# Kernel tuning notes

Measured on AMD Instinct MI355X. Metric: run time of the kernel, lower is better.

## Reference

```python
import jax, jax.numpy as jnp
import numpy as np

NEG_SLOPE = 0.2
EPS = 1e-16  # PyG softmax eps


def _gat_conv(x, src, dst, W, att_src, att_dst, bias, heads, out_ch):
    """PyG GATConv (eval mode, self-loops already appended, concat output)."""
    N = x.shape[0]
    xw = (x @ W).reshape(N, heads, out_ch)            # [N,H,C]
    a_src = jnp.sum(xw * att_src, axis=-1)            # [N,H]
    a_dst = jnp.sum(xw * att_dst, axis=-1)            # [N,H]
    e = jax.nn.leaky_relu(a_src[src] + a_dst[dst], NEG_SLOPE)  # [E,H]
    m = jax.ops.segment_max(e, dst, num_segments=N)   # [N,H] (self-loops -> no empty segs)
    e = jnp.exp(e - m[dst])
    denom = jax.ops.segment_sum(e, dst, num_segments=N)
    alpha = e / (denom[dst] + EPS)                    # [E,H]
    msg = xw[src] * alpha[:, :, None]                 # [E,H,C]
    out = jax.ops.segment_sum(msg, dst, num_segments=N)  # [N,H,C]
    return out.reshape(N, heads * out_ch) + bias


def setup_inputs() -> dict:
    key = jax.random.key(0)
    ks = jax.random.split(key, 12)
    N, E, F_in, H, C, NC = 20000, 320000, 512, 8, 64, 32
    x = jax.random.normal(ks[0], (N, F_in), dtype=jnp.float32)
    edge_index = jax.random.randint(ks[1], (2, E), 0, N, dtype=jnp.int64)
    g = lambda k, shape, fan: jax.random.normal(k, shape, dtype=jnp.float32) * (1.0 / np.sqrt(fan))
    return {
        "x": x,
        "edge_index": edge_index,
        "W1": g(ks[2], (F_in, H * C), F_in),
        "att_src1": g(ks[3], (H, C), C),
        "att_dst1": g(ks[4], (H, C), C),
        "b1": jnp.zeros((H * C,), dtype=jnp.float32),
        "W2": g(ks[5], (H * C, NC), H * C),
        "att_src2": g(ks[6], (1, NC), NC),
        "att_dst2": g(ks[7], (1, NC), NC),
        "b2": jnp.zeros((NC,), dtype=jnp.float32),
    }


def reference(x, edge_index, W1, att_src1, att_dst1, b1, W2, att_src2, att_dst2, b2):
    N = x.shape[0]
    H, C = att_src1.shape
    NC = att_src2.shape[1]
    # GATConv adds self-loops by default
    loops = jnp.arange(N, dtype=edge_index.dtype)
    src = jnp.concatenate([edge_index[0], loops])
    dst = jnp.concatenate([edge_index[1], loops])
    h = _gat_conv(x, src, dst, W1, att_src1, att_dst1, b1, H, C)
    h = jax.nn.elu(h)
    h = _gat_conv(h, src, dst, W2, att_src2, att_dst2, b2, 1, NC)
    return jax.nn.log_softmax(h, axis=1)
```

## Files before the change

kernel.cpp:

```cpp
#include <hip/hip_runtime.h>
#include <math.h>

#define NEG_SLOPE 0.2f
#define SM_EPS 1e-16f

typedef short short8 __attribute__((ext_vector_type(8)));
typedef float floatx4 __attribute__((ext_vector_type(4)));


__device__ inline unsigned short f2bf(float x) {
    unsigned int u = __float_as_uint(x);
    unsigned int r = (u + 0x7FFFu + ((u >> 16) & 1u)) >> 16;
    return (unsigned short)r;
}

__device__ inline float bf2f(unsigned short h) {
    return __uint_as_float(((unsigned int)h) << 16);
}

__device__ inline float bflo(unsigned int u) { return __uint_as_float(u << 16); }
__device__ inline float bfhi(unsigned int u) { return __uint_as_float(u & 0xFFFF0000u); }

__device__ __forceinline__ void gl_lds16(const unsigned short* g, unsigned short* l) {
    __builtin_amdgcn_global_load_lds(
        (const __attribute__((address_space(1))) unsigned int*)(g),
        (__attribute__((address_space(3))) unsigned int*)(l), 16, 0, 0);
}

__device__ inline void get_edge(const int* __restrict__ srcA, const int* __restrict__ dstA,
                                int e, int E, int& s, int& d) {
    if (e < E) { s = srcA[e]; d = dstA[e]; }
    else { s = e - E; d = e - E; }
}


__global__ __launch_bounds__(256) void k_prep(const float* __restrict__ x,
                                              unsigned short* __restrict__ xb,
                                              const float* __restrict__ W1,
                                              unsigned short* __restrict__ w1t,
                                              const float* __restrict__ W2,
                                              unsigned short* __restrict__ w2bt,
                                              const int* __restrict__ dstA,
                                              int E, int Ep,
                                              int* __restrict__ deg,
                                              int nblk_deg, int nblk_x) {
    __shared__ float tile[32][33];
    int bx = blockIdx.x;
    int t = threadIdx.x;
    if (bx < nblk_deg) {
        int e = bx * 256 + t;
        if (e < Ep) {
            int d = (e < E) ? dstA[e] : (e - E);
            atomicAdd(&deg[d], 1);
        }
    } else if (bx < nblk_deg + nblk_x) {
        int i = ((bx - nblk_deg) * 256 + t) * 4;
        float4 v = *(const float4*)(x + i);
        ushort4 o;
        o.x = f2bf(v.x); o.y = f2bf(v.y); o.z = f2bf(v.z); o.w = f2bf(v.w);
        *(ushort4*)(xb + i) = o;
    } else if (bx < nblk_deg + nblk_x + 256) {
        int b = bx - nblk_deg - nblk_x;
        int kb = (b & 15) * 32;
        int nb = (b >> 4) * 32;
        int tx = t & 31, ty = t >> 5;
        #pragma unroll
        for (int i = 0; i < 32; i += 8)
            tile[ty + i][tx] = W1[(size_t)(kb + ty + i) * 512 + nb + tx];
        __syncthreads();
        #pragma unroll
        for (int i = 0; i < 32; i += 8)
            w1t[(size_t)(nb + ty + i) * 512 + kb + tx] = f2bf(tile[tx][ty + i]);
    } else {
        int i = (bx - nblk_deg - nblk_x - 256) * 256 + t;
        int c = i >> 9, k = i & 511;
        w2bt[i] = f2bf(W2[k * 32 + c]);
    }
}


__global__ __launch_bounds__(256) void k_scan1(const int* __restrict__ deg, int* __restrict__ incl,
                                               int* __restrict__ part, int N) {
    __shared__ int sm[256];
    int t = threadIdx.x;
    int i = blockIdx.x * 256 + t;
    int v = (i < N) ? deg[i] : 0;
    sm[t] = v; __syncthreads();
    for (int o = 1; o < 256; o <<= 1) {
        int x = (t >= o) ? sm[t - o] : 0;
        __syncthreads();
        sm[t] += x;
        __syncthreads();
    }
    if (i < N) incl[i] = sm[t];
    if (t == 255) part[blockIdx.x] = sm[255];
}

__global__ __launch_bounds__(256) void k_scan3(const int* __restrict__ incl, const int* __restrict__ part,
                                               const int* __restrict__ deg, int* __restrict__ off,
                                               int* __restrict__ cursor, int N) {
    __shared__ int sm[256];
    int bx = blockIdx.x, t = threadIdx.x;
    int partial = 0;
    for (int i = t; i < bx; i += 256) partial += part[i];
    sm[t] = partial; __syncthreads();
    for (int o = 128; o > 0; o >>= 1) {
        if (t < o) sm[t] += sm[t + o];
        __syncthreads();
    }
    int base = sm[0];
    int i = bx * 256 + t;
    if (i >= N) return;
    int v = incl[i] + base;
    off[i + 1] = v;
    cursor[i] = v - deg[i];
    if (i == 0) off[0] = 0;
}

__global__ __launch_bounds__(256) void k_scatter(const int* __restrict__ srcA, const int* __restrict__ dstA,
                                                 int E, int Ep, int* __restrict__ cursor,
                                                 int* __restrict__ src_s) {
    int e = blockIdx.x * 256 + threadIdx.x;
    if (e >= Ep) return;
    int s, d; get_edge(srcA, dstA, e, E, s, d);
    int p = atomicAdd(&cursor[d], 1);
    src_s[p] = s;
}


__global__ __launch_bounds__(256) void k_gemm1_mfma(const unsigned short* __restrict__ A,
                                                    const unsigned short* __restrict__ Bt,
                                                    const float* __restrict__ att_s,
                                                    const float* __restrict__ att_d,
                                                    unsigned short* __restrict__ C,
                                                    float* __restrict__ a_sd,
                                                    float* __restrict__ a_dd, int M) {
    const int K = 512;
    __shared__ unsigned short As[128 * 32];
    __shared__ unsigned short Bs[128 * 32];
    int t = threadIdx.x;
    int lane = t & 63;
    int w = t >> 6;
    int row0 = blockIdx.x * 128;
    int col0 = blockIdx.y * 128;
    int wm = (w >> 1) * 64, wn = (w & 1) * 64;
    int l15 = lane & 15, q = lane >> 4;

    int mrow = t >> 2;
    int kk = (t & 3) * 8;
    unsigned short* ldsA0 = &As[w * 512];
    unsigned short* ldsA1 = &As[2048 + w * 512];
    unsigned short* ldsB0 = &Bs[w * 512];
    unsigned short* ldsB1 = &Bs[2048 + w * 512];

    floatx4 acc[4][4] = {};

    for (int k0 = 0; k0 < K; k0 += 32) {
        gl_lds16(A  + (size_t)(row0 + mrow) * K + k0 + kk,      ldsA0);
        gl_lds16(A  + (size_t)(row0 + 64 + mrow) * K + k0 + kk, ldsA1);
        gl_lds16(Bt + (size_t)(col0 + mrow) * K + k0 + kk,      ldsB0);
        gl_lds16(Bt + (size_t)(col0 + 64 + mrow) * K + k0 + kk, ldsB1);
        __syncthreads();
        short8 af[4], bfr[4];
        #pragma unroll
        for (int i = 0; i < 4; ++i)
            af[i] = *(const short8*)(&As[(wm + i * 16 + l15) * 32 + q * 8]);
        #pragma unroll
        for (int j = 0; j < 4; ++j)
            bfr[j] = *(const short8*)(&Bs[(wn + j * 16 + l15) * 32 + q * 8]);
        #pragma unroll
        for (int i = 0; i < 4; ++i)
            #pragma unroll
            for (int j = 0; j < 4; ++j)
                acc[i][j] = __builtin_amdgcn_mfma_f32_16x16x32_bf16(af[i], bfr[j], acc[i][j], 0, 0, 0);
        __syncthreads();
    }

    #pragma unroll
    for (int i = 0; i < 4; ++i) {
        #pragma unroll
        for (int p = 0; p < 4; ++p) {
            int r = row0 + wm + i * 16 + q * 4 + p;
            if (r < M) {
                #pragma unroll
                for (int j = 0; j < 4; ++j) {
                    int c = col0 + wn + j * 16 + l15;
                    C[(size_t)r * 512 + c] = f2bf(acc[i][j][p]);
                }
            }
        }
    }

    int hh = blockIdx.y * 2 + (w & 1);
    float asr[4], adr[4];
    #pragma unroll
    for (int j = 0; j < 4; ++j) {
        asr[j] = att_s[hh * 64 + j * 16 + l15];
        adr[j] = att_d[hh * 64 + j * 16 + l15];
    }
    #pragma unroll
    for (int i = 0; i < 4; ++i) {
        #pragma unroll
        for (int p = 0; p < 4; ++p) {
            float ds = 0.f, dd = 0.f;
            #pragma unroll
            for (int j = 0; j < 4; ++j) {
                ds = fmaf(acc[i][j][p], asr[j], ds);
                dd = fmaf(acc[i][j][p], adr[j], dd);
            }
            #pragma unroll
            for (int mk = 1; mk <= 8; mk <<= 1) {
                ds += __shfl_xor(ds, mk);
                dd += __shfl_xor(dd, mk);
            }
            int r = row0 + wm + i * 16 + q * 4 + p;
            if (l15 == 0 && r < M) {
                a_sd[r * 8 + hh] = ds;
                a_dd[r * 8 + hh] = dd;
            }
        }
    }
}


__global__ __launch_bounds__(256) void k_l1(const unsigned short* __restrict__ xw,
                                            const float* __restrict__ a_s,
                                            const float* __restrict__ a_d,
                                            const int* __restrict__ off,
                                            const int* __restrict__ src_s,
                                            const float* __restrict__ bias,
                                            unsigned short* __restrict__ hout, int N) {
    int wid = threadIdx.x >> 6, lane = threadIdx.x & 63;
    int n = blockIdx.x * 4 + wid;
    if (n >= N) return;
    int p0 = off[n], p1 = off[n + 1];
    int q = lane >> 3;
    int be = lane >> 3;
    int bh = lane & 7;
    float adb = a_d[n * 8 + bh];
    const size_t cbase = (size_t)8 * lane;

    float acc[8] = {};
    float s = 0.f;
    int p = p0;
    for (; p + 8 <= p1; p += 8) {
        int bsrc = src_s[p + be];
        float e = a_s[bsrc * 8 + bh] + adb;
        e = e > 0.f ? e : NEG_SLOPE * e;
        float w8 = __expf(e);
        #pragma unroll
        for (int j = 0; j < 8; ++j) {
            int sj = __shfl(bsrc, j * 8);
            float wj = __shfl(w8, j * 8 + q);
            const uint4 u = *(const uint4*)(xw + (size_t)sj * 512 + cbase);
            s += wj;
            acc[0] = fmaf(wj, bflo(u.x), acc[0]); acc[1] = fmaf(wj, bfhi(u.x), acc[1]);
            acc[2] = fmaf(wj, bflo(u.y), acc[2]); acc[3] = fmaf(wj, bfhi(u.y), acc[3]);
            acc[4] = fmaf(wj, bflo(u.z), acc[4]); acc[5] = fmaf(wj, bfhi(u.z), acc[5]);
            acc[6] = fmaf(wj, bflo(u.w), acc[6]); acc[7] = fmaf(wj, bfhi(u.w), acc[7]);
        }
    }
    if (p < p1) {
        int nb = p1 - p;
        int bsrc = src_s[p + (be < nb ? be : 0)];
        float e = a_s[bsrc * 8 + bh] + adb;
        e = e > 0.f ? e : NEG_SLOPE * e;
        float w8 = __expf(e);
        for (int j = 0; j < nb; ++j) {
            int sj = __shfl(bsrc, j * 8);
            float wj = __shfl(w8, j * 8 + q);
            const uint4 u = *(const uint4*)(xw + (size_t)sj * 512 + cbase);
            s += wj;
            acc[0] = fmaf(wj, bflo(u.x), acc[0]); acc[1] = fmaf(wj, bfhi(u.x), acc[1]);
            acc[2] = fmaf(wj, bflo(u.y), acc[2]); acc[3] = fmaf(wj, bfhi(u.y), acc[3]);
            acc[4] = fmaf(wj, bflo(u.z), acc[4]); acc[5] = fmaf(wj, bfhi(u.z), acc[5]);
            acc[6] = fmaf(wj, bflo(u.w), acc[6]); acc[7] = fmaf(wj, bfhi(u.w), acc[7]);
        }
    }

    float inv = 1.f / (s + SM_EPS);
    unsigned int ov[4];
    #pragma unroll
    for (int j = 0; j < 4; ++j) {
        float v0 = acc[2 * j] * inv     + bias[cbase + 2 * j];
        float v1 = acc[2 * j + 1] * inv + bias[cbase + 2 * j + 1];
        v0 = v0 > 0.f ? v0 : expm1f(v0);
        v1 = v1 > 0.f ? v1 : expm1f(v1);
        ov[j] = (unsigned int)f2bf(v0) | ((unsigned int)f2bf(v1) << 16);
    }
    *(uint4*)(hout + (size_t)n * 512 + cbase) = make_uint4(ov[0], ov[1], ov[2], ov[3]);
}


__global__ __launch_bounds__(256) void k_gemm2_mfma(const unsigned short* __restrict__ A,
                                                    const unsigned short* __restrict__ Bt,
                                                    const float* __restrict__ att_s,
                                                    const float* __restrict__ att_d,
                                                    unsigned short* __restrict__ O,
                                                    float* __restrict__ a_s, float* __restrict__ a_d,
                                                    int M) {
    const int K = 512;
    __shared__ unsigned short As[64 * 40];
    __shared__ unsigned short Bs[32 * 40];
    int t = threadIdx.x;
    int lane = t & 63;
    int w = t >> 6;
    int row0 = blockIdx.x * 64;
    int l15 = lane & 15, q = lane >> 4;

    floatx4 acc[2] = {};

    for (int k0 = 0; k0 < K; k0 += 32) {
        {
            int flat = t * 8;
            int m = flat >> 5, kk = flat & 31;
            uint4 va = make_uint4(0u, 0u, 0u, 0u);
            int gr = row0 + m;
            if (gr < M) va = *(const uint4*)(A + (size_t)gr * K + k0 + kk);
            *(uint4*)(&As[m * 40 + kk]) = va;
            if (t < 128) {
                int nn = t >> 2, kb = (t & 3) * 8;
                *(uint4*)(&Bs[nn * 40 + kb]) = *(const uint4*)(Bt + (size_t)nn * K + k0 + kb);
            }
        }
        __syncthreads();
        short8 af = *(const short8*)(&As[(w * 16 + l15) * 40 + q * 8]);
        short8 b0 = *(const short8*)(&Bs[(l15) * 40 + q * 8]);
        short8 b1 = *(const short8*)(&Bs[(16 + l15) * 40 + q * 8]);
        acc[0] = __builtin_amdgcn_mfma_f32_16x16x32_bf16(af, b0, acc[0], 0, 0, 0);
        acc[1] = __builtin_amdgcn_mfma_f32_16x16x32_bf16(af, b1, acc[1], 0, 0, 0);
        __syncthreads();
    }

    float as_lo = att_s[l15], as_hi = att_s[16 + l15];
    float ad_lo = att_d[l15], ad_hi = att_d[16 + l15];
    #pragma unroll
    for (int p = 0; p < 4; ++p) {
        int r = row0 + w * 16 + q * 4 + p;
        bool ok = r < M;
        float v0 = acc[0][p], v1 = acc[1][p];
        if (ok) {
            O[(size_t)r * 32 + l15]      = f2bf(v0);
            O[(size_t)r * 32 + 16 + l15] = f2bf(v1);
        }
        float ds = v0 * as_lo + v1 * as_hi;
        float dd = v0 * ad_lo + v1 * ad_hi;
        #pragma unroll
        for (int mk = 1; mk <= 8; mk <<= 1) {
            ds += __shfl_xor(ds, mk);
            dd += __shfl_xor(dd, mk);
        }
        if (ok && l15 == 0) { a_s[r] = ds; a_d[r] = dd; }
    }
}


__global__ __launch_bounds__(256) void k_l2(const unsigned short* __restrict__ hw2,
                                            const float* __restrict__ a_s,
                                            const float* __restrict__ a_d,
                                            const int* __restrict__ off,
                                            const int* __restrict__ src_s,
                                            const float* __restrict__ bias,
                                            float* __restrict__ outp, int N) {
    int wid = threadIdx.x >> 6, lane = threadIdx.x & 63;
    int n = blockIdx.x * 4 + wid;
    if (n >= N) return;
    int p0 = off[n], p1 = off[n + 1];
    float adv = a_d[n];
    int c = lane & 31, ep = lane >> 5;

    float acc = 0.f, s = 0.f;
    int p = p0;
    for (; p + 64 <= p1; p += 64) {
        int bsrc = src_s[p + lane];
        float e = a_s[bsrc] + adv;
        e = e > 0.f ? e : NEG_SLOPE * e;
        float w64 = __expf(e);
        #pragma unroll
        for (int j = 0; j < 64; j += 2) {
            int sj = __shfl(bsrc, j + ep);
            float wj = __shfl(w64, j + ep);
            s += wj;
            acc = fmaf(wj, bf2f(hw2[(size_t)sj * 32 + c]), acc);
        }
    }
    if (p < p1) {
        int nb = p1 - p;
        int bsrc = src_s[p + (lane < nb ? lane : 0)];
        float e = a_s[bsrc] + adv;
        e = e > 0.f ? e : NEG_SLOPE * e;
        float w64 = __expf(e);
        for (int j = 0; j < nb; j += 2) {
            int idx = j + ep;
            bool valid = idx < nb;
            int idc = valid ? idx : 0;
            int sj = __shfl(bsrc, idc);
            float wj = __shfl(w64, idc);
            if (valid) {
                s += wj;
                acc = fmaf(wj, bf2f(hw2[(size_t)sj * 32 + c]), acc);
            }
        }
    }
    acc += __shfl_xor(acc, 32);
    s   += __shfl_xor(s, 32);
    float v = acc / (s + SM_EPS) + bias[c];
    float mx = v;
    #pragma unroll
    for (int mk = 16; mk >= 1; mk >>= 1) mx = fmaxf(mx, __shfl_xor(mx, mk, 32));
    float ex = __expf(v - mx);
    float sum = ex;
    #pragma unroll
    for (int mk = 16; mk >= 1; mk >>= 1) sum += __shfl_xor(sum, mk, 32);
    if (lane < 32) outp[(size_t)n * 32 + c] = (v - mx) - __logf(sum);
}


extern "C" void kernel_launch(void* const* d_in, const int* in_sizes, int n_in,
                              void* d_out, int out_size, void* d_ws, size_t ws_size,
                              hipStream_t stream) {
    const float* x   = (const float*)d_in[0];
    const int*   ei  = (const int*)d_in[1];
    const float* W1  = (const float*)d_in[2];
    const float* as1 = (const float*)d_in[3];
    const float* ad1 = (const float*)d_in[4];
    const float* b1  = (const float*)d_in[5];
    const float* W2  = (const float*)d_in[6];
    const float* as2 = (const float*)d_in[7];
    const float* ad2 = (const float*)d_in[8];
    const float* b2  = (const float*)d_in[9];
    float* out = (float*)d_out;

    const int F = 512;
    const int N = in_sizes[0] / F;
    const int E = in_sizes[1] / 2;
    const int Ep = E + N;
    const int* srcA = ei;
    const int* dstA = ei + E;

    char* w = (char*)d_ws;
    auto alloc = [&](size_t b) -> void* {
        void* p = (void*)w;
        w += (b + 255) & ~(size_t)255;
        return p;
    };
    unsigned short* xbf  = (unsigned short*)alloc((size_t)N * 512 * 2);
    unsigned short* w1t  = (unsigned short*)alloc((size_t)512 * 512 * 2);
    unsigned short* w2bt = (unsigned short*)alloc((size_t)32 * 512 * 2);
    unsigned short* xw1  = (unsigned short*)alloc((size_t)N * 512 * 2);
    unsigned short* hbuf = (unsigned short*)alloc((size_t)N * 512 * 2);
    float* a_s1 = (float*)alloc((size_t)N * 8 * 4);
    float* a_d1 = (float*)alloc((size_t)N * 8 * 4);
    unsigned short* hw2 = (unsigned short*)alloc((size_t)N * 32 * 2);
    float* a_s2 = (float*)alloc((size_t)N * 4);
    float* a_d2 = (float*)alloc((size_t)N * 4);
    int* deg    = (int*)alloc((size_t)N * 4);
    int* incl   = (int*)alloc((size_t)N * 4);
    int* part   = (int*)alloc(256 * 4);
    int* off    = (int*)alloc((size_t)(N + 1) * 4);
    int* cursor = (int*)alloc((size_t)N * 4);
    int* src_s  = (int*)alloc((size_t)Ep * 4);

    int egrid = (Ep + 255) / 256;
    int sgrid = (N + 255) / 256;
    int ngrid4 = (N + 3) / 4;
    int nblk_x = (N * 512 / 4) / 256;
    int nblk_w2 = (32 * 512 + 255) / 256;

    hipMemsetAsync(deg, 0, (size_t)N * 4, stream);

    k_prep<<<egrid + nblk_x + 256 + nblk_w2, 256, 0, stream>>>(
        x, xbf, W1, w1t, W2, w2bt, dstA, E, Ep, deg, egrid, nblk_x);

    k_scan1<<<sgrid, 256, 0, stream>>>(deg, incl, part, N);
    k_scan3<<<sgrid, 256, 0, stream>>>(incl, part, deg, off, cursor, N);
    k_scatter<<<egrid, 256, 0, stream>>>(srcA, dstA, E, Ep, cursor, src_s);

    {
        dim3 g1((N + 127) / 128, 512 / 128);
        k_gemm1_mfma<<<g1, 256, 0, stream>>>(xbf, w1t, as1, ad1, xw1, a_s1, a_d1, N);
    }
    k_l1<<<ngrid4, 256, 0, stream>>>(xw1, a_s1, a_d1, off, src_s, b1, hbuf, N);

    k_gemm2_mfma<<<(N + 63) / 64, 256, 0, stream>>>(hbuf, w2bt, as2, ad2, hw2, a_s2, a_d2, N);
    k_l2<<<ngrid4, 256, 0, stream>>>(hw2, a_s2, a_d2, off, src_s, b2, out, N);
}
```

Baseline: 261.8 us.

## Split layer-1 aggregation per head with head-major attention scores

The attention logits a_s/a_d are now stored head-major ([H][N]) instead of node-major. The layer-1 aggregation kernel now gives each group of 8 lanes one (node, head) pair, with the head taken from blockIdx. Each lane computes its own edge weight and loads a 16-byte slice of the source row for that head, processing two edges per iteration. This removes the cross-lane shuffles and improves locality of the score gathers. In exchange, each edge's src index is loaded redundantly, each row gather is only 128 bytes per head group, and the per-lane edge loop is longer and more serial, so the load imbalance from varying degree grows.

```diff
diff --git a/kernel.cpp b/kernel.cpp
--- a/kernel.cpp
+++ b/kernel.cpp
@@ -215,8 +215,8 @@
             }
             int r = row0 + wm + i * 16 + q * 4 + p;
             if (l15 == 0 && r < M) {
-                a_sd[r * 8 + hh] = ds;
-                a_dd[r * 8 + hh] = dd;
+                a_sd[(size_t)hh * M + r] = ds;
+                a_dd[(size_t)hh * M + r] = dd;
             }
         }
     }
@@ -231,51 +231,47 @@
                                             const float* __restrict__ bias,
                                             unsigned short* __restrict__ hout, int N) {
     int wid = threadIdx.x >> 6, lane = threadIdx.x & 63;
-    int n = blockIdx.x * 4 + wid;
+    int h = blockIdx.x & 7;
+    int n = (blockIdx.x >> 3) * 32 + wid * 8 + (lane >> 3);
+    int li = lane & 7;
     if (n >= N) return;
     int p0 = off[n], p1 = off[n + 1];
-    int q = lane >> 3;
-    int be = lane >> 3;
-    int bh = lane & 7;
-    float adb = a_d[n * 8 + bh];
-    const size_t cbase = (size_t)8 * lane;
+    const float* ash = a_s + (size_t)h * N;
+    float adv = a_d[(size_t)h * N + n];
+    const size_t cbase = (size_t)h * 64 + (size_t)li * 8;
 
     float acc[8] = {};
     float s = 0.f;
     int p = p0;
-    for (; p + 8 <= p1; p += 8) {
-        int bsrc = src_s[p + be];
-        float e = a_s[bsrc * 8 + bh] + adb;
-        e = e > 0.f ? e : NEG_SLOPE * e;
-        float w8 = __expf(e);
-        #pragma unroll
-        for (int j = 0; j < 8; ++j) {
-            int sj = __shfl(bsrc, j * 8);
-            float wj = __shfl(w8, j * 8 + q);
-            const uint4 u = *(const uint4*)(xw + (size_t)sj * 512 + cbase);
-            s += wj;
-            acc[0] = fmaf(wj, bflo(u.x), acc[0]); acc[1] = fmaf(wj, bfhi(u.x), acc[1]);
-            acc[2] = fmaf(wj, bflo(u.y), acc[2]); acc[3] = fmaf(wj, bfhi(u.y), acc[3]);
-            acc[4] = fmaf(wj, bflo(u.z), acc[4]); acc[5] = fmaf(wj, bfhi(u.z), acc[5]);
-            acc[6] = fmaf(wj, bflo(u.w), acc[6]); acc[7] = fmaf(wj, bfhi(u.w), acc[7]);
-        }
+    for (; p + 2 <= p1; p += 2) {
+        int s0 = src_s[p];
+        int s1 = src_s[p + 1];
+        const uint4 u0 = *(const uint4*)(xw + (size_t)s0 * 512 + cbase);
+        const uint4 u1 = *(const uint4*)(xw + (size_t)s1 * 512 + cbase);
+        float e0 = ash[s0] + adv; e0 = e0 > 0.f ? e0 : NEG_SLOPE * e0;
+        float e1 = ash[s1] + adv; e1 = e1 > 0.f ? e1 : NEG_SLOPE * e1;
+        float w0 = __expf(e0);
+        float w1 = __expf(e1);
+        s += w0 + w1;
+        acc[0] = fmaf(w0, bflo(u0.x), acc[0]); acc[1] = fmaf(w0, bfhi(u0.x), acc[1]);
+        acc[2] = fmaf(w0, bflo(u0.y), acc[2]); acc[3] = fmaf(w0, bfhi(u0.y), acc[3]);
+        acc[4] = fmaf(w0, bflo(u0.z), acc[4]); acc[5] = fmaf(w0, bfhi(u0.z), acc[5]);
+        acc[6] = fmaf(w0, bflo(u0.w), acc[6]); acc[7] = fmaf(w0, bfhi(u0.w), acc[7]);
+        acc[0] = fmaf(w1, bflo(u1.x), acc[0]); acc[1] = fmaf(w1, bfhi(u1.x), acc[1]);
+        acc[2] = fmaf(w1, bflo(u1.y), acc[2]); acc[3] = fmaf(w1, bfhi(u1.y), acc[3]);
+        acc[4] = fmaf(w1, bflo(u1.z), acc[4]); acc[5] = fmaf(w1, bfhi(u1.z), acc[5]);
+        acc[6] = fmaf(w1, bflo(u1.w), acc[6]); acc[7] = fmaf(w1, bfhi(u1.w), acc[7]);
     }
     if (p < p1) {
-        int nb = p1 - p;
-        int bsrc = src_s[p + (be < nb ? be : 0)];
-        float e = a_s[bsrc * 8 + bh] + adb;
-        e = e > 0.f ? e : NEG_SLOPE * e;
-        float w8 = __expf(e);
-        for (int j = 0; j < nb; ++j) {
-            int sj = __shfl(bsrc, j * 8);
-            float wj = __shfl(w8, j * 8 + q);
-            const uint4 u = *(const uint4*)(xw + (size_t)sj * 512 + cbase);
-            s += wj;
-            acc[0] = fmaf(wj, bflo(u.x), acc[0]); acc[1] = fmaf(wj, bfhi(u.x), acc[1]);
-            acc[2] = fmaf(wj, bflo(u.y), acc[2]); acc[3] = fmaf(wj, bfhi(u.y), acc[3]);
-            acc[4] = fmaf(wj, bflo(u.z), acc[4]); acc[5] = fmaf(wj, bfhi(u.z), acc[5]);
-            acc[6] = fmaf(wj, bflo(u.w), acc[6]); acc[7] = fmaf(wj, bfhi(u.w), acc[7]);
-        }
+        int s0 = src_s[p];
+        const uint4 u0 = *(const uint4*)(xw + (size_t)s0 * 512 + cbase);
+        float e0 = ash[s0] + adv; e0 = e0 > 0.f ? e0 : NEG_SLOPE * e0;
+        float w0 = __expf(e0);
+        s += w0;
+        acc[0] = fmaf(w0, bflo(u0.x), acc[0]); acc[1] = fmaf(w0, bfhi(u0.x), acc[1]);
+        acc[2] = fmaf(w0, bflo(u0.y), acc[2]); acc[3] = fmaf(w0, bfhi(u0.y), acc[3]);
+        acc[4] = fmaf(w0, bflo(u0.z), acc[4]); acc[5] = fmaf(w0, bfhi(u0.z), acc[5]);
+        acc[6] = fmaf(w0, bflo(u0.w), acc[6]); acc[7] = fmaf(w0, bfhi(u0.w), acc[7]);
     }
 
     float inv = 1.f / (s + SM_EPS);
@@ -480,7 +476,10 @@
         dim3 g1((N + 127) / 128, 512 / 128);
         k_gemm1_mfma<<<g1, 256, 0, stream>>>(xbf, w1t, as1, ad1, xw1, a_s1, a_d1, N);
     }
-    k_l1<<<ngrid4, 256, 0, stream>>>(xw1, a_s1, a_d1, off, src_s, b1, hbuf, N);
+    {
+        int ngrid32 = (N + 31) / 32;
+        k_l1<<<ngrid32 * 8, 256, 0, stream>>>(xw1, a_s1, a_d1, off, src_s, b1, hbuf, N);
+    }
 
     k_gemm2_mfma<<<(N + 63) / 64, 256, 0, stream>>>(hbuf, w2bt, as2, ad2, hw2, a_s2, a_d2, N);
     k_l2<<<ngrid4, 256, 0, stream>>>(hw2, a_s2, a_d2, off, src_s, b2, out, N);
```

Result: faster. 250.9 us (-4.2%).
